# Kernel tuning notes

Hardware: AMD Instinct MI355X
Metric: run time of the kernel (lower is better)

Reference implementation:

```python
import jax, jax.numpy as jnp
import numpy as np

N_NODES = 50000
N_EDGES = 800000
D_IN = 64
D_RADIAL = 128


def setup_inputs() -> dict:
    key = jax.random.key(0)
    k1, k2, k3, k4, k5 = jax.random.split(key, 5)
    x = jax.random.normal(k1, (N_NODES, D_IN), dtype=jnp.float32)
    edge_basis = jax.random.normal(k2, (N_EDGES, D_RADIAL), dtype=jnp.float32)
    src = jax.random.randint(k3, (N_EDGES,), 0, N_NODES, dtype=jnp.int32)
    dst = jax.random.randint(k4, (N_EDGES,), 0, N_NODES, dtype=jnp.int32)
    # kaiming normal fan_in, linear nonlinearity: std = 1/sqrt(fan_in)
    W = jax.random.normal(k5, (D_IN, D_RADIAL), dtype=jnp.float32) / jnp.sqrt(
        jnp.float32(D_RADIAL))
    b = jnp.zeros((D_IN,), dtype=jnp.float32)
    return {"x": x, "edge_basis": edge_basis, "src": src, "dst": dst,
            "W": W, "b": b}


def reference(x, edge_basis, src, dst, W, b):
    # per-edge radial filter: Linear(d_radial -> d_in)  [E, d_in]
    filt = jnp.einsum('er,dr->ed', edge_basis, W) + b
    # gather source node features, multiply by filter  [E, d_in]
    m = x[src] * filt
    # scatter-sum messages into destination nodes      [N, d_in]
    h = jax.ops.segment_sum(m, dst, num_segments=x.shape[0])
    return h
```

## Files before the change

kernel.cpp:

```cpp
#include <hip/hip_runtime.h>

#define N_NODES  50000
#define N_EDGES  800000
#define D_IN     64
#define D_RADIAL 128
#define NTILES   (N_EDGES / 64)

typedef __bf16 bf16x8 __attribute__((ext_vector_type(8)));
typedef float  f32x4  __attribute__((ext_vector_type(4)));
typedef short  s16x8  __attribute__((ext_vector_type(8)));

__device__ inline unsigned int pack_bf16_pair(float lo, float hi) {
    return __builtin_amdgcn_perm(__float_as_uint(hi), __float_as_uint(lo), 0x07060302u);
}

__device__ inline unsigned short f2bf_rne(float f) {
    unsigned int u = __float_as_uint(f);
    u += 0x7FFFu + ((u >> 16) & 1u);
    return (unsigned short)(u >> 16);
}

constexpr size_t ws_align(size_t x) { return (x + 255) & ~(size_t)255; }
constexpr size_t WS_CNT  = 0;
constexpr size_t WS_OFF  = ws_align(WS_CNT  + (size_t)N_NODES * 4);
constexpr size_t WS_CUR  = ws_align(WS_OFF  + (size_t)(N_NODES + 1) * 4);
constexpr size_t WS_BSUM = ws_align(WS_CUR  + (size_t)N_NODES * 4);
constexpr size_t WS_RANK = ws_align(WS_BSUM + 512);
constexpr size_t WS_MSG  = ws_align(WS_RANK + (size_t)N_EDGES * 4);
constexpr size_t WS_REQUIRED = WS_MSG + (size_t)N_EDGES * D_IN * 2;

#define SCAN_B    512
#define SCAN_NBLK ((N_NODES + SCAN_B - 1) / SCAN_B)
static_assert(SCAN_NBLK <= 128, "scan_tops assumes <=128 blocks");

__global__ __launch_bounds__(256) void hist_kernel(const int* __restrict__ dst,
                                                   int* __restrict__ cnt) {
    int i = blockIdx.x * 256 + threadIdx.x;
    if (i < N_EDGES) atomicAdd(&cnt[dst[i]], 1);
}

__global__ __launch_bounds__(SCAN_B) void scan_block(const int* __restrict__ cnt,
                                                     int* __restrict__ offs,
                                                     int* __restrict__ bsum) {
    const int t = threadIdx.x, b = blockIdx.x;
    const int i = b * SCAN_B + t;
    int v = (i < N_NODES) ? cnt[i] : 0;
    __shared__ int s[SCAN_B];
    s[t] = v;
    __syncthreads();
    for (int o = 1; o < SCAN_B; o <<= 1) {
        int add = (t >= o) ? s[t - o] : 0;
        __syncthreads();
        s[t] += add;
        __syncthreads();
    }
    if (i < N_NODES) offs[i] = s[t];
    if (t == SCAN_B - 1) bsum[b] = s[t];
}

__global__ __launch_bounds__(128) void scan_tops(int* __restrict__ bsum) {
    const int t = threadIdx.x;
    __shared__ int s[128];
    int v = (t < SCAN_NBLK) ? bsum[t] : 0;
    s[t] = v;
    __syncthreads();
    for (int o = 1; o < 128; o <<= 1) {
        int add = (t >= o) ? s[t - o] : 0;
        __syncthreads();
        s[t] += add;
        __syncthreads();
    }
    if (t < SCAN_NBLK) bsum[t] = s[t] - v;
}

__global__ __launch_bounds__(SCAN_B) void finalize_off(const int* __restrict__ cnt,
                                                       int* __restrict__ offs,
                                                       const int* __restrict__ bsum,
                                                       int* __restrict__ cur) {
    const int i = blockIdx.x * SCAN_B + threadIdx.x;
    if (i < N_NODES) {
        int e = offs[i] - cnt[i] + bsum[blockIdx.x];
        offs[i] = e;
        cur[i]  = e;
    }
    if (i == 0) offs[N_NODES] = N_EDGES;
}

__global__ __launch_bounds__(256) void scatter_rank(const int* __restrict__ dst,
                                                    int* __restrict__ cur,
                                                    int* __restrict__ rank) {
    int i = blockIdx.x * 256 + threadIdx.x;
    if (i < N_EDGES) rank[i] = atomicAdd(&cur[dst[i]], 1);
}

__global__ __launch_bounds__(256) void msg_kernel(
    const float* __restrict__ x,
    const float* __restrict__ eb,
    const int*   __restrict__ src,
    const int*   __restrict__ rank,
    const float* __restrict__ W,
    const float* __restrict__ bias_p,
    unsigned short* __restrict__ msg)
{
    const int lane = threadIdx.x & 63;
    const int wv   = threadIdx.x >> 6;
    const int l15  = lane & 15;
    const int quad = lane >> 4;

    bf16x8 wfrag[4][4];
    #pragma unroll
    for (int nt = 0; nt < 4; ++nt) {
        const int d = nt * 16 + l15;
        #pragma unroll
        for (int kt = 0; kt < 4; ++kt) {
            const float* p = W + d * D_RADIAL + kt * 32 + quad * 8;
            s16x8 s;
            #pragma unroll
            for (int j = 0; j < 8; ++j) s[j] = (short)f2bf_rne(p[j]);
            wfrag[nt][kt] = __builtin_bit_cast(bf16x8, s);
        }
    }
    float bv[4];
    #pragma unroll
    for (int nt = 0; nt < 4; ++nt) bv[nt] = bias_p[nt * 16 + l15];

    for (int tile = blockIdx.x; tile < NTILES; tile += gridDim.x) {
        const int ebase = tile * 64 + wv * 16;
        const int erow  = ebase + quad * 4;

        int sv[4], rk[4];
        #pragma unroll
        for (int reg = 0; reg < 4; ++reg) {
            sv[reg] = src[erow + reg];
            rk[reg] = rank[erow + reg];
        }

        f32x4 acc[4];
        #pragma unroll
        for (int nt = 0; nt < 4; ++nt) acc[nt] = (f32x4){0.f, 0.f, 0.f, 0.f};

        #pragma unroll
        for (int kt = 0; kt < 4; ++kt) {
            const float* p = eb + (long)(ebase + l15) * D_RADIAL + kt * 32 + quad * 8;
            f32x4 a0 = *(const f32x4*)(p);
            f32x4 a1 = *(const f32x4*)(p + 4);
            int4 packed;
            packed.x = pack_bf16_pair(a0[0], a0[1]);
            packed.y = pack_bf16_pair(a0[2], a0[3]);
            packed.z = pack_bf16_pair(a1[0], a1[1]);
            packed.w = pack_bf16_pair(a1[2], a1[3]);
            bf16x8 afrag = __builtin_bit_cast(bf16x8, packed);
            #pragma unroll
            for (int nt = 0; nt < 4; ++nt)
                acc[nt] = __builtin_amdgcn_mfma_f32_16x16x32_bf16(
                    afrag, wfrag[nt][kt], acc[nt], 0, 0, 0);
        }

        #pragma unroll
        for (int reg = 0; reg < 4; ++reg) {
            const float*    xrow = x   + (long)sv[reg] * D_IN;
            unsigned short* mrow = msg + (long)rk[reg] * D_IN;
            #pragma unroll
            for (int nt = 0; nt < 4; ++nt) {
                const int d = nt * 16 + l15;
                mrow[d] = f2bf_rne((acc[nt][reg] + bv[nt]) * xrow[d]);
            }
        }
    }
}

__global__ __launch_bounds__(256) void gather_out(
    const unsigned short* __restrict__ msg,
    const int* __restrict__ offs,
    float* __restrict__ out)
{
    const int lane = threadIdx.x & 63;
    const int wid  = blockIdx.x * 4 + (threadIdx.x >> 6);
    const int wstr = gridDim.x * 4;
    for (int n = wid; n < N_NODES; n += wstr) {
        const int j0 = offs[n], j1 = offs[n + 1];
        const unsigned short* p = msg + (size_t)j0 * D_IN + lane;
        float a0 = 0.f, a1 = 0.f, a2 = 0.f, a3 = 0.f;
        int j = j0;
        for (; j + 4 <= j1; j += 4, p += 4 * D_IN) {
            a0 += __uint_as_float((unsigned int)p[0]        << 16);
            a1 += __uint_as_float((unsigned int)p[D_IN]     << 16);
            a2 += __uint_as_float((unsigned int)p[2 * D_IN] << 16);
            a3 += __uint_as_float((unsigned int)p[3 * D_IN] << 16);
        }
        for (; j < j1; ++j, p += D_IN)
            a0 += __uint_as_float((unsigned int)p[0] << 16);
        out[(size_t)n * D_IN + lane] = (a0 + a1) + (a2 + a3);
    }
}

__global__ __launch_bounds__(256) void edge_msg_kernel(
    const float* __restrict__ x,
    const float* __restrict__ eb,
    const int*   __restrict__ src,
    const int*   __restrict__ dst,
    const float* __restrict__ W,
    const float* __restrict__ bias_p,
    float*       __restrict__ out)
{
    const int lane = threadIdx.x & 63;
    const int wv   = threadIdx.x >> 6;
    const int l15  = lane & 15;
    const int quad = lane >> 4;

    bf16x8 wfrag[4][4];
    #pragma unroll
    for (int nt = 0; nt < 4; ++nt) {
        const int d = nt * 16 + l15;
        #pragma unroll
        for (int kt = 0; kt < 4; ++kt) {
            const float* p = W + d * D_RADIAL + kt * 32 + quad * 8;
            s16x8 s;
            #pragma unroll
            for (int j = 0; j < 8; ++j) s[j] = (short)f2bf_rne(p[j]);
            wfrag[nt][kt] = __builtin_bit_cast(bf16x8, s);
        }
    }
    float bv[4];
    #pragma unroll
    for (int nt = 0; nt < 4; ++nt) bv[nt] = bias_p[nt * 16 + l15];

    for (int tile = blockIdx.x; tile < NTILES; tile += gridDim.x) {
        const int ebase = tile * 64 + wv * 16;

        f32x4 acc[4];
        #pragma unroll
        for (int nt = 0; nt < 4; ++nt) acc[nt] = (f32x4){0.f, 0.f, 0.f, 0.f};

        #pragma unroll
        for (int kt = 0; kt < 4; ++kt) {
            const float* p = eb + (long)(ebase + l15) * D_RADIAL + kt * 32 + quad * 8;
            f32x4 a0 = *(const f32x4*)(p);
            f32x4 a1 = *(const f32x4*)(p + 4);
            int4 packed;
            packed.x = pack_bf16_pair(a0[0], a0[1]);
            packed.y = pack_bf16_pair(a0[2], a0[3]);
            packed.z = pack_bf16_pair(a1[0], a1[1]);
            packed.w = pack_bf16_pair(a1[2], a1[3]);
            bf16x8 afrag = __builtin_bit_cast(bf16x8, packed);
            #pragma unroll
            for (int nt = 0; nt < 4; ++nt)
                acc[nt] = __builtin_amdgcn_mfma_f32_16x16x32_bf16(
                    afrag, wfrag[nt][kt], acc[nt], 0, 0, 0);
        }

        const int erow = ebase + quad * 4;
        #pragma unroll
        for (int reg = 0; reg < 4; ++reg) {
            const int e  = erow + reg;
            const int sv = src[e];
            const int dv = dst[e];
            const float* xrow = x   + (long)sv * D_IN;
            float*       orow = out + (long)dv * D_IN;
            #pragma unroll
            for (int nt = 0; nt < 4; ++nt) {
                const int d = nt * 16 + l15;
                const float val = (acc[nt][reg] + bv[nt]) * xrow[d];
                unsafeAtomicAdd(orow + d, val);
            }
        }
    }
}

extern "C" void kernel_launch(void* const* d_in, const int* in_sizes, int n_in,
                              void* d_out, int out_size, void* d_ws, size_t ws_size,
                              hipStream_t stream) {
    const float* x    = (const float*)d_in[0];
    const float* eb   = (const float*)d_in[1];
    const int*   src  = (const int*)d_in[2];
    const int*   dst  = (const int*)d_in[3];
    const float* W    = (const float*)d_in[4];
    const float* bias = (const float*)d_in[5];
    float* out = (float*)d_out;

    if (ws_size >= WS_REQUIRED) {
        char* ws   = (char*)d_ws;
        int*  cnt  = (int*)(ws + WS_CNT);
        int*  offs = (int*)(ws + WS_OFF);
        int*  cur  = (int*)(ws + WS_CUR);
        int*  bsum = (int*)(ws + WS_BSUM);
        int*  rank = (int*)(ws + WS_RANK);
        unsigned short* msg = (unsigned short*)(ws + WS_MSG);

        hipMemsetAsync(cnt, 0, (size_t)N_NODES * 4, stream);
        hist_kernel  <<<(N_EDGES + 255) / 256, 256, 0, stream>>>(dst, cnt);
        scan_block   <<<SCAN_NBLK, SCAN_B, 0, stream>>>(cnt, offs, bsum);
        scan_tops    <<<1, 128, 0, stream>>>(bsum);
        finalize_off <<<SCAN_NBLK, SCAN_B, 0, stream>>>(cnt, offs, bsum, cur);
        scatter_rank <<<(N_EDGES + 255) / 256, 256, 0, stream>>>(dst, cur, rank);
        msg_kernel   <<<1280, 256, 0, stream>>>(x, eb, src, rank, W, bias, msg);
        gather_out   <<<1024, 256, 0, stream>>>(msg, offs, out);
    } else {
        hipMemsetAsync(d_out, 0, (size_t)N_NODES * D_IN * sizeof(float), stream);
        edge_msg_kernel<<<1024, 256, 0, stream>>>(x, eb, src, dst, W, bias, out);
    }
}
```

Before: 697.5 us.

## Write messages in edge order and gather them via a sorted edge-index permutation

Previously msg_kernel scattered each bf16 message row to its destination-sorted rank, which gives random 2-byte writes. Now messages are written contiguously in edge order with nontemporal stores, and scatter_order builds a permutation (order) that gather_out uses to read message rows indirectly. This makes the large write coalesced but turns the gather's contiguous reads into random row reads plus an extra index load per edge. The atomic counting pass now writes scattered edge indices instead of ranks.

```diff
diff --git a/kernel.cpp b/kernel.cpp
--- a/kernel.cpp
+++ b/kernel.cpp
@@ -25,8 +25,8 @@
 constexpr size_t WS_OFF  = ws_align(WS_CNT  + (size_t)N_NODES * 4);
 constexpr size_t WS_CUR  = ws_align(WS_OFF  + (size_t)(N_NODES + 1) * 4);
 constexpr size_t WS_BSUM = ws_align(WS_CUR  + (size_t)N_NODES * 4);
-constexpr size_t WS_RANK = ws_align(WS_BSUM + 512);
-constexpr size_t WS_MSG  = ws_align(WS_RANK + (size_t)N_EDGES * 4);
+constexpr size_t WS_ORD  = ws_align(WS_BSUM + 512);
+constexpr size_t WS_MSG  = ws_align(WS_ORD  + (size_t)N_EDGES * 4);
 constexpr size_t WS_REQUIRED = WS_MSG + (size_t)N_EDGES * D_IN * 2;
 
 #define SCAN_B    512
@@ -86,18 +86,17 @@
     if (i == 0) offs[N_NODES] = N_EDGES;
 }
 
-__global__ __launch_bounds__(256) void scatter_rank(const int* __restrict__ dst,
-                                                    int* __restrict__ cur,
-                                                    int* __restrict__ rank) {
+__global__ __launch_bounds__(256) void scatter_order(const int* __restrict__ dst,
+                                                     int* __restrict__ cur,
+                                                     int* __restrict__ order) {
     int i = blockIdx.x * 256 + threadIdx.x;
-    if (i < N_EDGES) rank[i] = atomicAdd(&cur[dst[i]], 1);
+    if (i < N_EDGES) order[atomicAdd(&cur[dst[i]], 1)] = i;
 }
 
 __global__ __launch_bounds__(256) void msg_kernel(
     const float* __restrict__ x,
     const float* __restrict__ eb,
     const int*   __restrict__ src,
-    const int*   __restrict__ rank,
     const float* __restrict__ W,
     const float* __restrict__ bias_p,
     unsigned short* __restrict__ msg)
@@ -128,12 +127,9 @@
         const int ebase = tile * 64 + wv * 16;
         const int erow  = ebase + quad * 4;
 
-        int sv[4], rk[4];
-        #pragma unroll
-        for (int reg = 0; reg < 4; ++reg) {
-            sv[reg] = src[erow + reg];
-            rk[reg] = rank[erow + reg];
-        }
+        int sv[4];
+        #pragma unroll
+        for (int reg = 0; reg < 4; ++reg) sv[reg] = src[erow + reg];
 
         f32x4 acc[4];
         #pragma unroll
@@ -159,11 +155,12 @@
         #pragma unroll
         for (int reg = 0; reg < 4; ++reg) {
             const float*    xrow = x   + (long)sv[reg] * D_IN;
-            unsigned short* mrow = msg + (long)rk[reg] * D_IN;
+            unsigned short* mrow = msg + (long)(erow + reg) * D_IN;
             #pragma unroll
             for (int nt = 0; nt < 4; ++nt) {
                 const int d = nt * 16 + l15;
-                mrow[d] = f2bf_rne((acc[nt][reg] + bv[nt]) * xrow[d]);
+                __builtin_nontemporal_store(
+                    f2bf_rne((acc[nt][reg] + bv[nt]) * xrow[d]), mrow + d);
             }
         }
     }
@@ -171,6 +168,7 @@
 
 __global__ __launch_bounds__(256) void gather_out(
     const unsigned short* __restrict__ msg,
+    const int* __restrict__ order,
     const int* __restrict__ offs,
     float* __restrict__ out)
 {
@@ -179,17 +177,18 @@
     const int wstr = gridDim.x * 4;
     for (int n = wid; n < N_NODES; n += wstr) {
         const int j0 = offs[n], j1 = offs[n + 1];
-        const unsigned short* p = msg + (size_t)j0 * D_IN + lane;
         float a0 = 0.f, a1 = 0.f, a2 = 0.f, a3 = 0.f;
         int j = j0;
-        for (; j + 4 <= j1; j += 4, p += 4 * D_IN) {
-            a0 += __uint_as_float((unsigned int)p[0]        << 16);
-            a1 += __uint_as_float((unsigned int)p[D_IN]     << 16);
-            a2 += __uint_as_float((unsigned int)p[2 * D_IN] << 16);
-            a3 += __uint_as_float((unsigned int)p[3 * D_IN] << 16);
-        }
-        for (; j < j1; ++j, p += D_IN)
-            a0 += __uint_as_float((unsigned int)p[0] << 16);
+        for (; j + 4 <= j1; j += 4) {
+            const long r0 = order[j],     r1 = order[j + 1];
+            const long r2 = order[j + 2], r3 = order[j + 3];
+            a0 += __uint_as_float((unsigned int)msg[r0 * D_IN + lane] << 16);
+            a1 += __uint_as_float((unsigned int)msg[r1 * D_IN + lane] << 16);
+            a2 += __uint_as_float((unsigned int)msg[r2 * D_IN + lane] << 16);
+            a3 += __uint_as_float((unsigned int)msg[r3 * D_IN + lane] << 16);
+        }
+        for (; j < j1; ++j)
+            a0 += __uint_as_float((unsigned int)msg[(long)order[j] * D_IN + lane] << 16);
         out[(size_t)n * D_IN + lane] = (a0 + a1) + (a2 + a3);
     }
 }
@@ -284,17 +283,17 @@
         int*  offs = (int*)(ws + WS_OFF);
         int*  cur  = (int*)(ws + WS_CUR);
         int*  bsum = (int*)(ws + WS_BSUM);
-        int*  rank = (int*)(ws + WS_RANK);
+        int*  order = (int*)(ws + WS_ORD);
         unsigned short* msg = (unsigned short*)(ws + WS_MSG);
 
         hipMemsetAsync(cnt, 0, (size_t)N_NODES * 4, stream);
-        hist_kernel  <<<(N_EDGES + 255) / 256, 256, 0, stream>>>(dst, cnt);
-        scan_block   <<<SCAN_NBLK, SCAN_B, 0, stream>>>(cnt, offs, bsum);
-        scan_tops    <<<1, 128, 0, stream>>>(bsum);
-        finalize_off <<<SCAN_NBLK, SCAN_B, 0, stream>>>(cnt, offs, bsum, cur);
-        scatter_rank <<<(N_EDGES + 255) / 256, 256, 0, stream>>>(dst, cur, rank);
-        msg_kernel   <<<1280, 256, 0, stream>>>(x, eb, src, rank, W, bias, msg);
-        gather_out   <<<1024, 256, 0, stream>>>(msg, offs, out);
+        hist_kernel   <<<(N_EDGES + 255) / 256, 256, 0, stream>>>(dst, cnt);
+        scan_block    <<<SCAN_NBLK, SCAN_B, 0, stream>>>(cnt, offs, bsum);
+        scan_tops     <<<1, 128, 0, stream>>>(bsum);
+        finalize_off  <<<SCAN_NBLK, SCAN_B, 0, stream>>>(cnt, offs, bsum, cur);
+        scatter_order <<<(N_EDGES + 255) / 256, 256, 0, stream>>>(dst, cur, order);
+        msg_kernel    <<<1280, 256, 0, stream>>>(x, eb, src, W, bias, msg);
+        gather_out    <<<1024, 256, 0, stream>>>(msg, order, offs, out);
     } else {
         hipMemsetAsync(d_out, 0, (size_t)N_NODES * D_IN * sizeof(float), stream);
         edge_msg_kernel<<<1024, 256, 0, stream>>>(x, eb, src, dst, W, bias, out);
```

Measured after the change: 752.0 us. +7.8%, slower.
